# Kernel optimization log

Measured on AMD Instinct MI355X. Metric: run time of the kernel, lower is better.

## Reference

```python
import jax, jax.numpy as jnp
import numpy as np

D_MODEL = 512
SCALE = 1.0 / (D_MODEL ** 0.5)  # module scales by 1/sqrt(d_model), not d_head
NEG = -1000000000.0

def setup_inputs() -> dict:
    key = jax.random.key(0)
    kq, kk, kv, kl = jax.random.split(key, 4)
    B, H, S, Dh = 4, 8, 2048, 64
    Q = jax.random.normal(kq, (B, H, S, Dh), dtype=jnp.float32)
    K = jax.random.normal(kk, (B, H, S, Dh), dtype=jnp.float32)
    V = jax.random.normal(kv, (B, H, S, Dh), dtype=jnp.float32)
    src_batch_lens = jax.random.randint(kl, (B,), 1, S + 1, dtype=jnp.int32)
    return {"Q": Q, "K": K, "V": V, "src_batch_lens": src_batch_lens}

def reference(Q, K, V, src_batch_lens):
    # scores: [B, H, Sq, Sk]
    scores = jnp.einsum('bhqd,bhkd->bhqk', Q, K) * SCALE
    Sk = K.shape[2]
    # mask keys at positions >= per-batch length
    key_mask = jnp.arange(Sk)[None, None, None, :] >= src_batch_lens[:, None, None, None]
    scores = jnp.where(key_mask, NEG, scores)
    attn = jax.nn.softmax(scores, axis=-1)
    # dropout is identity in eval/reference (p=0)
    context = jnp.einsum('bhqk,bhkd->bhqd', attn, V)
    return context
```

## Files before the change

kernel.cpp:

```cpp
#include <hip/hip_runtime.h>


#define S_LEN 2048
#define DH 64
#define QK_SCALE ((float)(1.4426950408889634 / 22.627416997969522))

typedef __attribute__((ext_vector_type(8))) short bf16x8;
typedef __attribute__((ext_vector_type(4))) float f32x4;

__device__ __forceinline__ short f2bf(float f) {
    __bf16 h = (__bf16)f;
    return __builtin_bit_cast(short, h);
}

#define SW(r, e) ((e) ^ (((r) & 7) << 3))

__global__ __launch_bounds__(256, 2)
void attn_fwd(const float* __restrict__ Qg, const float* __restrict__ Kg,
              const float* __restrict__ Vg, const int* __restrict__ lens,
              float* __restrict__ Og)
{
    __shared__ short Klds[2][64][64];
    __shared__ short Vt[2][64][64];
    __shared__ short Plds[4][16][64];

    const int tid  = threadIdx.x;
    const int wave = tid >> 6;
    const int lane = tid & 63;
    const int lr   = lane & 15;
    const int lg   = lane >> 4;

    const int bh = ((blockIdx.y & 3) << 3) | (blockIdx.y >> 2);
    const int L  = lens[bh >> 3];
    const int q0 = blockIdx.x * 64 + wave * 16;
    const size_t base = (size_t)bh * S_LEN * DH;

    bf16x8 qf[2];
    {
        const float* qrow = Qg + base + (size_t)(q0 + lr) * DH + 8 * lg;
        #pragma unroll
        for (int ks = 0; ks < 2; ++ks) {
            float4 a = *(const float4*)(qrow + 32 * ks);
            float4 b = *(const float4*)(qrow + 32 * ks + 4);
            bf16x8 f;
            f[0] = f2bf(a.x * QK_SCALE); f[1] = f2bf(a.y * QK_SCALE);
            f[2] = f2bf(a.z * QK_SCALE); f[3] = f2bf(a.w * QK_SCALE);
            f[4] = f2bf(b.x * QK_SCALE); f[5] = f2bf(b.y * QK_SCALE);
            f[6] = f2bf(b.z * QK_SCALE); f[7] = f2bf(b.w * QK_SCALE);
            qf[ks] = f;
        }
    }

    f32x4 Of[4];
    #pragma unroll
    for (int n = 0; n < 4; ++n) Of[n] = (f32x4){0.f, 0.f, 0.f, 0.f};
    f32x4 Dsum = (f32x4){0.f, 0.f, 0.f, 0.f};
    bf16x8 ones;
    #pragma unroll
    for (int j = 0; j < 8; ++j) ones[j] = (short)0x3F80;

    const int ntiles = (L + 63) >> 6;

    const int krow = tid >> 3;
    const int kc8  = (tid & 7) * 8;

    float4 kreg[4];
    float  vreg[16];

    {
        const float* kt = Kg + base;
        #pragma unroll
        for (int p = 0; p < 2; ++p) {
            kreg[2 * p]     = *(const float4*)(kt + (krow + 32 * p) * DH + kc8);
            kreg[2 * p + 1] = *(const float4*)(kt + (krow + 32 * p) * DH + kc8 + 4);
        }
        const float* vt = Vg + base;
        #pragma unroll
        for (int i = 0; i < 16; ++i)
            vreg[i] = vt[(wave * 16 + i) * DH + lane];
    }
    {
        #pragma unroll
        for (int p = 0; p < 2; ++p) {
            int row = krow + 32 * p;
            bf16x8 s;
            s[0] = f2bf(kreg[2*p].x); s[1] = f2bf(kreg[2*p].y);
            s[2] = f2bf(kreg[2*p].z); s[3] = f2bf(kreg[2*p].w);
            s[4] = f2bf(kreg[2*p+1].x); s[5] = f2bf(kreg[2*p+1].y);
            s[6] = f2bf(kreg[2*p+1].z); s[7] = f2bf(kreg[2*p+1].w);
            *(bf16x8*)&Klds[0][row][SW(row, kc8)] = s;
        }
        bf16x8 a, b;
        #pragma unroll
        for (int i = 0; i < 8; ++i) { a[i] = f2bf(vreg[i]); b[i] = f2bf(vreg[8 + i]); }
        *(bf16x8*)&Vt[0][lane][SW(lane, wave * 16)]     = a;
        *(bf16x8*)&Vt[0][lane][SW(lane, wave * 16 + 8)] = b;
    }
    __syncthreads();

    for (int t = 0; t < ntiles; ++t) {
        const int cur = t & 1;
        const int kb = t * 64;
        const bool pre = (t + 1 < ntiles);

        if (pre) {
            const float* kt = Kg + base + (size_t)(kb + 64) * DH;
            #pragma unroll
            for (int p = 0; p < 2; ++p) {
                kreg[2 * p]     = *(const float4*)(kt + (krow + 32 * p) * DH + kc8);
                kreg[2 * p + 1] = *(const float4*)(kt + (krow + 32 * p) * DH + kc8 + 4);
            }
            const float* vt = Vg + base + (size_t)(kb + 64) * DH;
            #pragma unroll
            for (int i = 0; i < 16; ++i)
                vreg[i] = vt[(wave * 16 + i) * DH + lane];
        }

        f32x4 Sv[4];
        #pragma unroll
        for (int n = 0; n < 4; ++n) Sv[n] = (f32x4){0.f, 0.f, 0.f, 0.f};
        #pragma unroll
        for (int ks = 0; ks < 2; ++ks) {
            #pragma unroll
            for (int n = 0; n < 4; ++n) {
                bf16x8 kf = *(const bf16x8*)&Klds[cur][16 * n + lr][SW(16 * n + lr, 8 * lg + 32 * ks)];
                Sv[n] = __builtin_amdgcn_mfma_f32_16x16x32_bf16(kf, qf[ks], Sv[n], 0, 0, 0);
            }
        }

        if (kb + 64 > L) {
            #pragma unroll
            for (int n = 0; n < 4; ++n) {
                const int kbase = kb + 16 * n + 4 * lg;
                #pragma unroll
                for (int r = 0; r < 4; ++r)
                    if (kbase + r >= L) Sv[n][r] = -1e30f;
            }
        }

        #pragma unroll
        for (int n = 0; n < 4; ++n) {
            short4 pq;
            pq.x = f2bf(exp2f(Sv[n][0]));
            pq.y = f2bf(exp2f(Sv[n][1]));
            pq.z = f2bf(exp2f(Sv[n][2]));
            pq.w = f2bf(exp2f(Sv[n][3]));
            *(short4*)&Plds[wave][lr][SW(lr, 16 * n + 4 * lg)] = pq;
        }

        #pragma unroll
        for (int ks = 0; ks < 2; ++ks) {
            bf16x8 pf = *(const bf16x8*)&Plds[wave][lr][SW(lr, 8 * lg + 32 * ks)];
            Dsum = __builtin_amdgcn_mfma_f32_16x16x32_bf16(pf, ones, Dsum, 0, 0, 0);
            #pragma unroll
            for (int n = 0; n < 4; ++n) {
                bf16x8 vf = *(const bf16x8*)&Vt[cur][16 * n + lr][SW(16 * n + lr, 8 * lg + 32 * ks)];
                Of[n] = __builtin_amdgcn_mfma_f32_16x16x32_bf16(pf, vf, Of[n], 0, 0, 0);
            }
        }

        if (pre) {
            const int b = cur ^ 1;
            #pragma unroll
            for (int p = 0; p < 2; ++p) {
                int row = krow + 32 * p;
                bf16x8 s;
                s[0] = f2bf(kreg[2*p].x); s[1] = f2bf(kreg[2*p].y);
                s[2] = f2bf(kreg[2*p].z); s[3] = f2bf(kreg[2*p].w);
                s[4] = f2bf(kreg[2*p+1].x); s[5] = f2bf(kreg[2*p+1].y);
                s[6] = f2bf(kreg[2*p+1].z); s[7] = f2bf(kreg[2*p+1].w);
                *(bf16x8*)&Klds[b][row][SW(row, kc8)] = s;
            }
            bf16x8 a, bb;
            #pragma unroll
            for (int i = 0; i < 8; ++i) { a[i] = f2bf(vreg[i]); bb[i] = f2bf(vreg[8 + i]); }
            *(bf16x8*)&Vt[b][lane][SW(lane, wave * 16)]     = a;
            *(bf16x8*)&Vt[b][lane][SW(lane, wave * 16 + 8)] = bb;
        }
        __syncthreads();
    }

    float inv[4];
    #pragma unroll
    for (int r = 0; r < 4; ++r) inv[r] = 1.f / Dsum[r];
    float* orow = Og + base + (size_t)q0 * DH;
    #pragma unroll
    for (int r = 0; r < 4; ++r) {
        int q = 4 * lg + r;
        #pragma unroll
        for (int n = 0; n < 4; ++n)
            orow[(size_t)q * DH + 16 * n + lr] = Of[n][r] * inv[r];
    }
}

extern "C" void kernel_launch(void* const* d_in, const int* in_sizes, int n_in,
                              void* d_out, int out_size, void* d_ws, size_t ws_size,
                              hipStream_t stream) {
    const float* Q = (const float*)d_in[0];
    const float* K = (const float*)d_in[1];
    const float* V = (const float*)d_in[2];
    const int* lens = (const int*)d_in[3];
    float* O = (float*)d_out;
    dim3 grid(S_LEN / 64, 4 * 8);
    attn_fwd<<<grid, 256, 0, stream>>>(Q, K, V, lens, O);
}
```

Baseline: 139.1 us.

## Keep P in registers by permuting V key rows to match MFMA output layout

Removes the per-wave LDS round trip for the softmax probabilities. The exp2 results of the QK^T MFMA are packed straight into bf16x8 A-operands for the PV MFMA. To keep the key ordering consistent, each V row is loaded from a permuted key index (vkey) so the transposed V tile in LDS matches the register layout of P. This saves LDS writes and reads and the LDS space for P, at the cost of a less regular global V access pattern.

New measurement: 137.0 us. Within noise of the previous version (-1.5%).

```diff
diff --git a/kernel.cpp b/kernel.cpp
--- a/kernel.cpp
+++ b/kernel.cpp
@@ -22,7 +22,6 @@
 {
     __shared__ short Klds[2][64][64];
     __shared__ short Vt[2][64][64];
-    __shared__ short Plds[4][16][64];
 
     const int tid  = threadIdx.x;
     const int wave = tid >> 6;
@@ -64,6 +63,12 @@
     const int krow = tid >> 3;
     const int kc8  = (tid & 7) * 8;
 
+    int vkey[16];
+    #pragma unroll
+    for (int i = 0; i < 16; ++i)
+        vkey[i] = 16 * (wave & ~1) + (((i >> 2) & 1) << 4) + ((wave & 1) << 3)
+                + ((i >> 3) << 2) + (i & 3);
+
     float4 kreg[4];
     float  vreg[16];
 
@@ -77,7 +82,7 @@
         const float* vt = Vg + base;
         #pragma unroll
         for (int i = 0; i < 16; ++i)
-            vreg[i] = vt[(wave * 16 + i) * DH + lane];
+            vreg[i] = vt[vkey[i] * DH + lane];
     }
     {
         #pragma unroll
@@ -113,7 +118,7 @@
             const float* vt = Vg + base + (size_t)(kb + 64) * DH;
             #pragma unroll
             for (int i = 0; i < 16; ++i)
-                vreg[i] = vt[(wave * 16 + i) * DH + lane];
+                vreg[i] = vt[vkey[i] * DH + lane];
         }
 
         f32x4 Sv[4];
@@ -138,24 +143,24 @@
             }
         }
 
-        #pragma unroll
-        for (int n = 0; n < 4; ++n) {
-            short4 pq;
-            pq.x = f2bf(exp2f(Sv[n][0]));
-            pq.y = f2bf(exp2f(Sv[n][1]));
-            pq.z = f2bf(exp2f(Sv[n][2]));
-            pq.w = f2bf(exp2f(Sv[n][3]));
-            *(short4*)&Plds[wave][lr][SW(lr, 16 * n + 4 * lg)] = pq;
-        }
-
-        #pragma unroll
-        for (int ks = 0; ks < 2; ++ks) {
-            bf16x8 pf = *(const bf16x8*)&Plds[wave][lr][SW(lr, 8 * lg + 32 * ks)];
-            Dsum = __builtin_amdgcn_mfma_f32_16x16x32_bf16(pf, ones, Dsum, 0, 0, 0);
+        bf16x8 pf[2];
+        #pragma unroll
+        for (int ks = 0; ks < 2; ++ks) {
+            #pragma unroll
+            for (int h = 0; h < 2; ++h) {
+                #pragma unroll
+                for (int r = 0; r < 4; ++r)
+                    pf[ks][4 * h + r] = f2bf(exp2f(Sv[2 * ks + h][r]));
+            }
+        }
+
+        #pragma unroll
+        for (int ks = 0; ks < 2; ++ks) {
+            Dsum = __builtin_amdgcn_mfma_f32_16x16x32_bf16(pf[ks], ones, Dsum, 0, 0, 0);
             #pragma unroll
             for (int n = 0; n < 4; ++n) {
                 bf16x8 vf = *(const bf16x8*)&Vt[cur][16 * n + lr][SW(16 * n + lr, 8 * lg + 32 * ks)];
-                Of[n] = __builtin_amdgcn_mfma_f32_16x16x32_bf16(pf, vf, Of[n], 0, 0, 0);
+                Of[n] = __builtin_amdgcn_mfma_f32_16x16x32_bf16(pf[ks], vf, Of[n], 0, 0, 0);
             }
         }
 
```
